# Optimization experiments

Measured on AMD Instinct MI355X. Metric: run time of the kernel, lower is better.

## Reference

```python
import jax, jax.numpy as jnp
import numpy as np


def _nearest_resize(x, Hl, Wl):
    # x: [B, Hf, Wf] -> [B, Hl, Wl], PyTorch F.interpolate(mode='nearest') semantics:
    # src_idx = floor(out_idx * in_size / out_size)
    B, Hf, Wf = x.shape
    ri = (jnp.arange(Hl) * Hf) // Hl
    ci = (jnp.arange(Wl) * Wf) // Wl
    return x[:, ri[:, None], ci[None, :]]


def _nearest_centroid(f, c):
    # f: [B, C, H, W], c: [K, C]
    # argmin_k ||f - c_k||_2 over channels == argmin of squared distance
    f2 = jnp.sum(f * f, axis=1)                       # [B, H, W]
    c2 = jnp.sum(c * c, axis=1)                       # [K]
    cross = jnp.einsum('bchw,kc->bkhw', f, c)         # [B, K, H, W]
    d2 = f2[:, None] - 2.0 * cross + c2[None, :, None, None]
    return jnp.argmin(d2, axis=1)                     # [B, H, W] int


def setup_inputs() -> dict:
    key = jax.random.key(0)
    k1, k2, k3, k4, k5, k6 = jax.random.split(key, 6)
    B, C, Hf, Wf = 4, 256, 64, 128
    K = 19  # class_num
    Hl, Wl = 512, 1024
    return {
        'feature_s2t': jax.random.normal(k1, (B, C, Hf, Wf), dtype=jnp.float32),
        'feature_target': jax.random.normal(k2, (B, C, Hf, Wf), dtype=jnp.float32),
        'label_s2t': jax.random.randint(k3, (B, Hl, Wl), 0, K, dtype=jnp.int64) if jax.config.jax_enable_x64 else jax.random.randint(k3, (B, Hl, Wl), 0, K, dtype=jnp.int32),
        'label_target': jax.random.randint(k4, (B, Hl, Wl), 0, K, dtype=jnp.int32),
        'centroid_s2t': jax.random.normal(k5, (K, C), dtype=jnp.float32),
        'centroid_target': jax.random.normal(k6, (K, C), dtype=jnp.float32),
    }


def reference(feature_s2t, feature_target, label_s2t, label_target, centroid_s2t, centroid_target):
    # feature_s2t is matched against the TARGET-domain centroids and vice versa
    # (cross assignment, exactly as in the torch forward).
    mask_s2t = _nearest_centroid(feature_s2t, centroid_target)     # [B, Hf, Wf]
    mask_target = _nearest_centroid(feature_target, centroid_s2t)  # [B, Hf, Wf]
    Hl, Wl = label_s2t.shape[1], label_s2t.shape[2]
    mask_s2t = _nearest_resize(mask_s2t, Hl, Wl).astype(jnp.int32)
    Hl2, Wl2 = label_target.shape[1], label_target.shape[2]
    mask_target = _nearest_resize(mask_target, Hl2, Wl2).astype(jnp.int32)
    return (mask_s2t, mask_target)
```

## Files before the change

### kernel.cpp

```cpp
#include <hip/hip_runtime.h>

#define K   19
#define C   256
#define HF  64
#define WF  128
#define HW  (HF * WF)
#define BB  4
#define HL  512
#define WL  1024

#define TAU 0.015f

__global__ __launch_bounds__(256, 4) void centroid_mask_kernel(
    const float* __restrict__ feat0,
    const float* __restrict__ feat1,
    const float* __restrict__ cent0,
    const float* __restrict__ cent1,
    int* __restrict__ out)
{
    __shared__ float  part[4 * K * 64];
    __shared__ double c2p[K][8];
    __shared__ double sc2d[K];
    __shared__ float  sc2f[K];

    const int map = blockIdx.y;
    const float* __restrict__ feat = (map == 0) ? feat0 : feat1;
    const float* __restrict__ cent = (map == 0) ? cent0 : cent1;

    const int tid  = threadIdx.x;
    const int lane = tid & 63;
    const int wv   = __builtin_amdgcn_readfirstlane(tid >> 6);

    if (tid < K * 8) {
        const int k = tid >> 3, sl = tid & 7;
        const float* cp = cent + k * C + sl * 32;
        double s = 0.0;
        #pragma unroll
        for (int j = 0; j < 32; ++j) { double v = (double)cp[j]; s = fma(v, v, s); }
        c2p[k][sl] = s;
    }

    const int p  = blockIdx.x * 64 + lane;
    const int hw = p & (HW - 1);
    const int b  = p >> 13;
    const int cb = wv * 64;

    const float* __restrict__ fp = feat + (size_t)b * C * HW + (size_t)cb * HW + hw;
    const float* __restrict__ cw = cent + cb;

    float acc[K];
    #pragma unroll
    for (int k = 0; k < K; ++k) acc[k] = 0.f;

    #pragma unroll
    for (int ch = 0; ch < 8; ++ch) {
        float f8[8];
        #pragma unroll
        for (int i = 0; i < 8; ++i)
            f8[i] = fp[(size_t)(ch * 8 + i) * HW];
        #pragma unroll
        for (int k = 0; k < K; ++k) {
            const float* __restrict__ ck = cw + (size_t)k * C + ch * 8;
            float a = acc[k];
            a = fmaf(f8[0], ck[0], a); a = fmaf(f8[1], ck[1], a);
            a = fmaf(f8[2], ck[2], a); a = fmaf(f8[3], ck[3], a);
            a = fmaf(f8[4], ck[4], a); a = fmaf(f8[5], ck[5], a);
            a = fmaf(f8[6], ck[6], a); a = fmaf(f8[7], ck[7], a);
            acc[k] = a;
        }
    }

    float* __restrict__ pw = &part[(wv * K) * 64 + lane];
    #pragma unroll
    for (int k = 0; k < K; ++k) pw[k * 64] = acc[k];
    __syncthreads();

    if (tid < K) {
        double s = 0.0;
        #pragma unroll
        for (int j = 0; j < 8; ++j) s += c2p[tid][j];
        sc2d[tid] = s;
        sc2f[tid] = (float)s;
    }
    __syncthreads();

    if (tid < 64) {
        const int pix = tid;
        float d[K];
        #pragma unroll
        for (int k = 0; k < K; ++k) {
            const float s = (part[(0 * K + k) * 64 + pix] + part[(1 * K + k) * 64 + pix])
                          + (part[(2 * K + k) * 64 + pix] + part[(3 * K + k) * 64 + pix]);
            d[k] = sc2f[k] - 2.0f * s;
        }
        int best = 0; float m1 = d[0];
        #pragma unroll
        for (int k = 1; k < K; ++k) if (d[k] < m1) { m1 = d[k]; best = k; }

        unsigned cmask = 0u;
        #pragma unroll
        for (int k = 0; k < K; ++k) if (d[k] - m1 < TAU) cmask |= (1u << k);

        const bool need = (cmask & (cmask - 1)) != 0u;
        unsigned long long ball = __ballot(need);
        while (ball) {
            const int px = (int)__builtin_ctzll(ball);
            ball &= ball - 1;
            const unsigned pm  = __shfl(cmask, px, 64);
            const int      phw = __shfl(hw,    px, 64);
            const int      pb  = __shfl(b,     px, 64);
            const float* __restrict__ fcol = feat + (size_t)pb * C * HW + phw;

            const int c0 = tid << 2;
            double pf[4];
            #pragma unroll
            for (int j = 0; j < 4; ++j)
                pf[j] = (double)fcol[(size_t)(c0 + j) * HW];

            double bd = 1e300; int bi = 0;
            unsigned mm = pm;
            while (mm) {
                const int k = (int)__builtin_ctz(mm);
                mm &= mm - 1;
                const float* __restrict__ ck = cent + (size_t)k * C + c0;
                double s = 0.0;
                #pragma unroll
                for (int j = 0; j < 4; ++j)
                    s = fma(pf[j], (double)ck[j], s);
                #pragma unroll
                for (int off = 1; off < 64; off <<= 1)
                    s += __shfl_xor(s, off, 64);
                const double dk = sc2d[k] - 2.0 * s;
                if (dk < bd) { bd = dk; bi = k; }
            }
            if (tid == px) best = bi;
        }

        const int w = hw & (WF - 1);
        const int h = hw >> 7;
        int4 v = make_int4(best, best, best, best);
        int* __restrict__ ob = out + (size_t)map * (BB * HL * WL)
                                   + (size_t)b * (HL * WL)
                                   + (size_t)(h * 8) * WL + (size_t)(w * 8);
        #pragma unroll
        for (int r = 0; r < 8; ++r) {
            *(int4*)(ob + (size_t)r * WL)     = v;
            *(int4*)(ob + (size_t)r * WL + 4) = v;
        }
    }
}

extern "C" void kernel_launch(void* const* d_in, const int* in_sizes, int n_in,
                              void* d_out, int out_size, void* d_ws, size_t ws_size,
                              hipStream_t stream) {
    const float* feature_s2t     = (const float*)d_in[0];
    const float* feature_target  = (const float*)d_in[1];
    const float* centroid_s2t    = (const float*)d_in[4];
    const float* centroid_target = (const float*)d_in[5];
    int* out = (int*)d_out;

    dim3 grid(32768 / 64, 2);
    dim3 block(256);
    hipLaunchKernelGGL(centroid_mask_kernel, grid, block, 0, stream,
                       feature_s2t, feature_target,
                       centroid_target, centroid_s2t, out);
}
```

Measured before the change: 25.38 us.

## Compute centroid dot products with split-bf16 MFMA instead of scalar FMAs

Replaces the per-thread fp32 FMA loop over 19 centroids with 32x32x16 bf16 MFMA instructions, using a hi/lo bf16 split of features and centroids (three products) to approximate fp32 accuracy. Centroids are split into bf16 halves in shared memory, and the per-wave partial results are reduced through a padded shared buffer. The near-tie threshold for the fp64 refinement pass is doubled to cover the added rounding error, which may send more pixels down the slow exact path.

Result: faster. 22.72 us (-10.5%).

```diff
diff --git a/kernel.cpp b/kernel.cpp
--- a/kernel.cpp
+++ b/kernel.cpp
@@ -9,7 +9,13 @@
 #define HL  512
 #define WL  1024
 
-#define TAU 0.015f
+#define TAU 0.03f
+
+#define CPAD 264
+#define DPAD 66
+
+typedef __attribute__((ext_vector_type(8)))  short bf16x8;
+typedef __attribute__((ext_vector_type(16))) float f32x16;
 
 __global__ __launch_bounds__(256, 4) void centroid_mask_kernel(
     const float* __restrict__ feat0,
@@ -18,7 +24,9 @@
     const float* __restrict__ cent1,
     int* __restrict__ out)
 {
-    __shared__ float  part[4 * K * 64];
+    __shared__ __align__(16) unsigned short chi[K * CPAD];
+    __shared__ __align__(16) unsigned short clo[K * CPAD];
+    __shared__ float  dbuf[2][2][16][DPAD];
     __shared__ double c2p[K][8];
     __shared__ double sc2d[K];
     __shared__ float  sc2f[K];
@@ -31,6 +39,13 @@
     const int lane = tid & 63;
     const int wv   = __builtin_amdgcn_readfirstlane(tid >> 6);
 
+    for (int i = tid; i < K * C; i += 256) {
+        const int k = i >> 8, c = i & (C - 1);
+        const unsigned u = __float_as_uint(cent[i]);
+        const float r = __uint_as_float(u) - __uint_as_float(u & 0xffff0000u);
+        chi[k * CPAD + c] = (unsigned short)(u >> 16);
+        clo[k * CPAD + c] = (unsigned short)(__float_as_uint(r) >> 16);
+    }
     if (tid < K * 8) {
         const int k = tid >> 3, sl = tid & 7;
         const float* cp = cent + k * C + sl * 32;
@@ -39,42 +54,7 @@
         for (int j = 0; j < 32; ++j) { double v = (double)cp[j]; s = fma(v, v, s); }
         c2p[k][sl] = s;
     }
-
-    const int p  = blockIdx.x * 64 + lane;
-    const int hw = p & (HW - 1);
-    const int b  = p >> 13;
-    const int cb = wv * 64;
-
-    const float* __restrict__ fp = feat + (size_t)b * C * HW + (size_t)cb * HW + hw;
-    const float* __restrict__ cw = cent + cb;
-
-    float acc[K];
-    #pragma unroll
-    for (int k = 0; k < K; ++k) acc[k] = 0.f;
-
-    #pragma unroll
-    for (int ch = 0; ch < 8; ++ch) {
-        float f8[8];
-        #pragma unroll
-        for (int i = 0; i < 8; ++i)
-            f8[i] = fp[(size_t)(ch * 8 + i) * HW];
-        #pragma unroll
-        for (int k = 0; k < K; ++k) {
-            const float* __restrict__ ck = cw + (size_t)k * C + ch * 8;
-            float a = acc[k];
-            a = fmaf(f8[0], ck[0], a); a = fmaf(f8[1], ck[1], a);
-            a = fmaf(f8[2], ck[2], a); a = fmaf(f8[3], ck[3], a);
-            a = fmaf(f8[4], ck[4], a); a = fmaf(f8[5], ck[5], a);
-            a = fmaf(f8[6], ck[6], a); a = fmaf(f8[7], ck[7], a);
-            acc[k] = a;
-        }
-    }
-
-    float* __restrict__ pw = &part[(wv * K) * 64 + lane];
-    #pragma unroll
-    for (int k = 0; k < K; ++k) pw[k * 64] = acc[k];
     __syncthreads();
-
     if (tid < K) {
         double s = 0.0;
         #pragma unroll
@@ -82,15 +62,70 @@
         sc2d[tid] = s;
         sc2f[tid] = (float)s;
     }
+
+    const int tile = wv >> 1, kh = wv & 1;
+    const int hl2  = (lane >> 5) & 1;
+    const int pp   = blockIdx.x * 64 + tile * 32 + (lane & 31);
+    const int hw   = pp & (HW - 1);
+    const int b    = pp >> 13;
+
+    const float* __restrict__ fp = feat + (size_t)b * C * HW + hw;
+    const int cb0  = kh * 128 + hl2 * 8;
+    const int bidx = min(lane & 31, 18) * CPAD + kh * 128 + hl2 * 8;
+
+    f32x16 acc;
+    #pragma unroll
+    for (int r = 0; r < 16; ++r) acc[r] = 0.f;
+
+    #pragma unroll
+    for (int s = 0; s < 8; ++s) {
+        const int cb = cb0 + s * 16;
+        float fv[8];
+        #pragma unroll
+        for (int j = 0; j < 8; ++j)
+            fv[j] = fp[(size_t)(cb + j) * HW];
+
+        union { unsigned u[4]; bf16x8 v; } ah, al, bh, bl;
+        #pragma unroll
+        for (int j = 0; j < 4; ++j) {
+            const unsigned u0 = __float_as_uint(fv[2*j]);
+            const unsigned u1 = __float_as_uint(fv[2*j+1]);
+            ah.u[j] = (u0 >> 16) | (u1 & 0xffff0000u);
+            const float r0 = fv[2*j]   - __uint_as_float(u0 & 0xffff0000u);
+            const float r1 = fv[2*j+1] - __uint_as_float(u1 & 0xffff0000u);
+            al.u[j] = (__float_as_uint(r0) >> 16)
+                    | (__float_as_uint(r1) & 0xffff0000u);
+        }
+        bh.v = *(const bf16x8*)&chi[bidx + s * 16];
+        bl.v = *(const bf16x8*)&clo[bidx + s * 16];
+
+        acc = __builtin_amdgcn_mfma_f32_32x32x16_bf16(ah.v, bh.v, acc, 0, 0, 0);
+        acc = __builtin_amdgcn_mfma_f32_32x32x16_bf16(ah.v, bl.v, acc, 0, 0, 0);
+        acc = __builtin_amdgcn_mfma_f32_32x32x16_bf16(al.v, bh.v, acc, 0, 0, 0);
+    }
+
+    {
+        float* dst = &dbuf[tile][kh][0][hl2 * 32 + (lane & 31)];
+        #pragma unroll
+        for (int r = 0; r < 16; ++r) dst[r * DPAD] = acc[r];
+    }
     __syncthreads();
 
     if (tid < 64) {
-        const int pix = tid;
+        const int l   = tid;
+        const int tl  = l >> 5, px = l & 31;
+        const int h   = (px >> 2) & 1;
+        const int reg = (px & 3) | ((px >> 3) << 2);
+        const int bse = h * 32;
+
+        const int ppx = blockIdx.x * 64 + l;
+        const int phw = ppx & (HW - 1);
+        const int pb  = ppx >> 13;
+
         float d[K];
         #pragma unroll
         for (int k = 0; k < K; ++k) {
-            const float s = (part[(0 * K + k) * 64 + pix] + part[(1 * K + k) * 64 + pix])
-                          + (part[(2 * K + k) * 64 + pix] + part[(3 * K + k) * 64 + pix]);
+            const float s = dbuf[tl][0][reg][bse + k] + dbuf[tl][1][reg][bse + k];
             d[k] = sc2f[k] - 2.0f * s;
         }
         int best = 0; float m1 = d[0];
@@ -104,12 +139,12 @@
         const bool need = (cmask & (cmask - 1)) != 0u;
         unsigned long long ball = __ballot(need);
         while (ball) {
-            const int px = (int)__builtin_ctzll(ball);
+            const int sx = (int)__builtin_ctzll(ball);
             ball &= ball - 1;
-            const unsigned pm  = __shfl(cmask, px, 64);
-            const int      phw = __shfl(hw,    px, 64);
-            const int      pb  = __shfl(b,     px, 64);
-            const float* __restrict__ fcol = feat + (size_t)pb * C * HW + phw;
+            const unsigned pm  = __shfl(cmask, sx, 64);
+            const int      fhw = __shfl(phw,   sx, 64);
+            const int      fb  = __shfl(pb,    sx, 64);
+            const float* __restrict__ fcol = feat + (size_t)fb * C * HW + fhw;
 
             const int c0 = tid << 2;
             double pf[4];
@@ -133,15 +168,15 @@
                 const double dk = sc2d[k] - 2.0 * s;
                 if (dk < bd) { bd = dk; bi = k; }
             }
-            if (tid == px) best = bi;
-        }
-
-        const int w = hw & (WF - 1);
-        const int h = hw >> 7;
+            if (tid == sx) best = bi;
+        }
+
+        const int w = phw & (WF - 1);
+        const int hh = phw >> 7;
         int4 v = make_int4(best, best, best, best);
         int* __restrict__ ob = out + (size_t)map * (BB * HL * WL)
-                                   + (size_t)b * (HL * WL)
-                                   + (size_t)(h * 8) * WL + (size_t)(w * 8);
+                                   + (size_t)pb * (HL * WL)
+                                   + (size_t)(hh * 8) * WL + (size_t)(w * 8);
         #pragma unroll
         for (int r = 0; r < 8; ++r) {
             *(int4*)(ob + (size_t)r * WL)     = v;
```
